# Kernel optimization log

Measured on AMD Instinct MI355X. Metric: run time of the kernel, lower is better.

## Reference

```python
import jax, jax.numpy as jnp
import numpy as np

EPS = 1e-08

def setup_inputs() -> dict:
    key = jax.random.key(0)
    ks = jax.random.split(key, 5)
    B, T, D, L = 8, 4096, 1024, 24
    data = jax.random.normal(ks[0], (B, T, D), dtype=jnp.float32)
    W_enc = jax.random.normal(ks[1], (L, D), dtype=jnp.float32) * (1.0 / np.sqrt(D))
    b_enc = jax.random.normal(ks[2], (L,), dtype=jnp.float32) * 0.01
    W_dec = jax.random.normal(ks[3], (D, L), dtype=jnp.float32) * (1.0 / np.sqrt(L))
    b_dec = jax.random.normal(ks[4], (D,), dtype=jnp.float32) * 0.01
    ecs = jnp.array([0.1], dtype=jnp.float32)  # error_correction_strength
    ep = jnp.array([1.0], dtype=jnp.float32)   # energy_preservation
    return {"data": data, "W_enc": W_enc, "b_enc": b_enc,
            "W_dec": W_dec, "b_dec": b_dec,
            "error_correction_strength": ecs, "energy_preservation": ep}

def _l2(x):
    return jnp.linalg.norm(x, axis=-1, keepdims=True)

def reference(data, W_enc, b_enc, W_dec, b_dec, error_correction_strength, energy_preservation):
    ecs = error_correction_strength[0]
    ep = energy_preservation[0]
    # --- encode_to_lattice ---
    in_e = _l2(data)                                   # [B,T,1]
    proj = jnp.einsum('btd,ld->btl', data, W_enc) + b_enc
    lattice_points = jnp.round(proj / ecs) * ecs       # quantize to lattice grid
    out_e = _l2(lattice_points)
    lattice = lattice_points * (in_e / (out_e + EPS)) * ep
    # --- decode_from_lattice ---
    in_e2 = _l2(lattice)
    corrected = jnp.where(jnp.abs(lattice) > ecs, lattice, 0.0)
    res = jnp.einsum('btl,dl->btd', corrected, W_dec) + b_dec
    out_e2 = _l2(res)
    return res * (in_e2 / (out_e2 + EPS)) * ep
```

## Files before the change

kernel.cpp:

```cpp
#include <hip/hip_runtime.h>
#include <math.h>

#define EPS 1e-8f

__global__ void prep_all(const float* __restrict__ W_enc,
                         const float* __restrict__ Wd, const float* __restrict__ bd,
                         float* __restrict__ wt, float* __restrict__ G,
                         float* __restrict__ h, float* __restrict__ bb) {
    int b = blockIdx.x;
    int lane = threadIdx.x;
    if (b < 384) {
        int i = b * 64 + lane;
        int k = i / 24, l = i - k * 24;
        wt[i] = W_enc[l * 1024 + k];
        return;
    }
    b -= 384;
    float s = 0.f;
    if (b < 576) {
        int l = b / 24, m = b - (b / 24) * 24;
        for (int d = lane; d < 1024; d += 64) s = fmaf(Wd[d * 24 + l], Wd[d * 24 + m], s);
    } else if (b < 600) {
        int l = b - 576;
        for (int d = lane; d < 1024; d += 64) s = fmaf(Wd[d * 24 + l], bd[d], s);
    } else {
        for (int d = lane; d < 1024; d += 64) s = fmaf(bd[d], bd[d], s);
    }
    for (int off = 32; off; off >>= 1) s += __shfl_down(s, off);
    if (lane == 0) {
        if (b < 576) G[b] = s;
        else if (b < 600) h[b - 576] = s;
        else *bb = s;
    }
}


constexpr int LD_TILE = 33;
constexpr int TILE_F  = 64 * LD_TILE;
constexpr int SMEM_F  = 4 * TILE_F;

__global__ __launch_bounds__(256, 4)
void leech_main(const float* __restrict__ data,
                const float* __restrict__ b_enc,
                const float* __restrict__ Wd,
                const float* __restrict__ b_dec,
                const float* __restrict__ ecs_p,
                const float* __restrict__ ep_p,
                const float* __restrict__ wt,
                const float* __restrict__ G,
                const float* __restrict__ h,
                const float* __restrict__ bbp,
                float* __restrict__ out)
{
    __shared__ float smem[SMEM_F];
    const int tid = threadIdx.x;
    const int w = tid >> 6;
    const int r = tid & 63;
    const int rowbase = blockIdx.x * 64;

    float* tile = smem + w * TILE_F;

    const int lrow = r >> 3;
    const int lk   = (r & 7) * 4;

    float proj[24];
#pragma unroll
    for (int l = 0; l < 24; ++l) proj[l] = 0.f;
    float ssq = 0.f;

    const int kw = __builtin_amdgcn_readfirstlane((tid >> 6) * 256);

    float4 buf[8];
#pragma unroll
    for (int it = 0; it < 8; ++it)
        buf[it] = *reinterpret_cast<const float4*>(
            data + (size_t)(rowbase + it * 8 + lrow) * 1024 + kw + lk);

    for (int sc = 0; sc < 8; ++sc) {
#pragma unroll
        for (int it = 0; it < 8; ++it) {
            float* t = tile + (it * 8 + lrow) * LD_TILE + lk;
            t[0] = buf[it].x; t[1] = buf[it].y; t[2] = buf[it].z; t[3] = buf[it].w;
        }
        if (sc < 7) {
            const int k0n = kw + (sc + 1) * 32;
#pragma unroll
            for (int it = 0; it < 8; ++it)
                buf[it] = *reinterpret_cast<const float4*>(
                    data + (size_t)(rowbase + it * 8 + lrow) * 1024 + k0n + lk);
        }
        const float* xrow = tile + r * LD_TILE;
        const int kofs = __builtin_amdgcn_readfirstlane(kw + sc * 32);
#pragma unroll 8
        for (int kk = 0; kk < 32; ++kk) {
            const float x = xrow[kk];
            ssq = fmaf(x, x, ssq);
            const float* wp = wt + (size_t)(kofs + kk) * 24;
#pragma unroll
            for (int l = 0; l < 24; ++l)
                proj[l] = fmaf(wp[l], x, proj[l]);
        }
    }

#pragma unroll
    for (int l = 0; l < 24; ++l)
        smem[w * TILE_F + l * 64 + r] = proj[l];
    smem[w * TILE_F + 24 * 64 + r] = ssq;
    __syncthreads();

    float p[24];
#pragma unroll
    for (int l = 0; l < 24; ++l)
        p[l] = (smem[0 * TILE_F + l * 64 + r] + smem[1 * TILE_F + l * 64 + r]) +
               (smem[2 * TILE_F + l * 64 + r] + smem[3 * TILE_F + l * 64 + r]);
    const float ss = (smem[0 * TILE_F + 24 * 64 + r] + smem[1 * TILE_F + 24 * 64 + r]) +
                     (smem[2 * TILE_F + 24 * 64 + r] + smem[3 * TILE_F + 24 * 64 + r]);
    __syncthreads();

    const float ecs = ecs_p[0];
    const float ep  = ep_p[0];
    const float in_e = sqrtf(ss);

    float lp[24]; float oe = 0.f;
#pragma unroll
    for (int l = 0; l < 24; ++l) {
        const float pp = p[l] + b_enc[l];
        const float q = rintf(pp / ecs) * ecs;
        lp[l] = q;
        oe = fmaf(q, q, oe);
    }
    const float s1 = in_e / (sqrtf(oe) + EPS) * ep;

    float c[24]; float ie = 0.f;
#pragma unroll
    for (int l = 0; l < 24; ++l) {
        const float lat = lp[l] * s1;
        ie = fmaf(lat, lat, ie);
        c[l] = (fabsf(lat) > ecs) ? lat : 0.f;
    }
    const float in_e2 = sqrtf(ie);

    float qacc = bbp[0];
#pragma unroll
    for (int l = 0; l < 24; ++l) {
        float s = 2.f * h[l];
#pragma unroll
        for (int m = 0; m < 24; ++m)
            s = fmaf(G[l * 24 + m], c[m], s);
        qacc = fmaf(s, c[l], qacc);
    }
    const float out_e2 = sqrtf(fmaxf(qacc, 0.f));
    const float s2 = in_e2 / (out_e2 + EPS) * ep;

    for (int sc = 0; sc < 8; ++sc) {
        const int d0 = __builtin_amdgcn_readfirstlane(kw + sc * 32);
        float* trow = tile + r * LD_TILE;
#pragma unroll 4
        for (int dd = 0; dd < 32; ++dd) {
            const int d = d0 + dd;
            const float* wr = Wd + d * 24;
            float acc = b_dec[d];
#pragma unroll
            for (int l = 0; l < 24; ++l)
                acc = fmaf(wr[l], c[l], acc);
            trow[dd] = acc * s2;
        }
#pragma unroll
        for (int it = 0; it < 8; ++it) {
            const float* t = tile + (it * 8 + lrow) * LD_TILE + lk;
            float4 v; v.x = t[0]; v.y = t[1]; v.z = t[2]; v.w = t[3];
            *reinterpret_cast<float4*>(
                out + (size_t)(rowbase + it * 8 + lrow) * 1024 + d0 + lk) = v;
        }
    }
}


extern "C" void kernel_launch(void* const* d_in, const int* in_sizes, int n_in,
                              void* d_out, int out_size, void* d_ws, size_t ws_size,
                              hipStream_t stream) {
    const float* data  = (const float*)d_in[0];
    const float* W_enc = (const float*)d_in[1];
    const float* b_enc = (const float*)d_in[2];
    const float* W_dec = (const float*)d_in[3];
    const float* b_dec = (const float*)d_in[4];
    const float* ecs   = (const float*)d_in[5];
    const float* ep    = (const float*)d_in[6];
    float* out = (float*)d_out;

    float* ws = (float*)d_ws;
    float* wt = ws;
    float* G  = ws + 24576;
    float* h  = ws + 25152;
    float* bb = ws + 25176;

    const int rows = in_sizes[0] / 1024;

    hipLaunchKernelGGL(prep_all, dim3(985), dim3(64), 0, stream,
                       W_enc, W_dec, b_dec, wt, G, h, bb);
    hipLaunchKernelGGL(leech_main, dim3(rows / 64), dim3(256), 0, stream,
                       data, b_enc, W_dec, b_dec, ecs, ep, wt, G, h, bb, out);
}
```

Baseline: 324.4 us.

## Split rows across eight waves, XOR-swizzle LDS tiles, use nontemporal output stores

Each 64-row block now uses 8 waves of 512 threads, with each wave covering 128 columns instead of 256. This halves the per-wave serial K loop and the decode loop, at the cost of a bigger cross-wave reduction. The padded LDS tile (stride 33) becomes an unpadded stride-32 tile with an XOR swizzle to avoid bank conflicts while keeping the footprint small. Output stores become nontemporal to avoid polluting the cache with streamed results. Launch bounds of 512x4 may raise register pressure given the 24-element accumulators.

```diff
diff --git a/kernel.cpp b/kernel.cpp
--- a/kernel.cpp
+++ b/kernel.cpp
@@ -2,6 +2,8 @@
 #include <math.h>
 
 #define EPS 1e-8f
+
+typedef float vfloat4 __attribute__((ext_vector_type(4)));
 
 __global__ void prep_all(const float* __restrict__ W_enc,
                          const float* __restrict__ Wd, const float* __restrict__ bd,
@@ -35,11 +37,12 @@
 }
 
 
-constexpr int LD_TILE = 33;
+constexpr int LD_TILE = 32;
 constexpr int TILE_F  = 64 * LD_TILE;
-constexpr int SMEM_F  = 4 * TILE_F;
-
-__global__ __launch_bounds__(256, 4)
+constexpr int NW      = 8;
+constexpr int SMEM_F  = NW * TILE_F;
+
+__global__ __launch_bounds__(512, 4)
 void leech_main(const float* __restrict__ data,
                 const float* __restrict__ b_enc,
                 const float* __restrict__ Wd,
@@ -68,7 +71,7 @@
     for (int l = 0; l < 24; ++l) proj[l] = 0.f;
     float ssq = 0.f;
 
-    const int kw = __builtin_amdgcn_readfirstlane((tid >> 6) * 256);
+    const int kw = __builtin_amdgcn_readfirstlane((tid >> 6) * 128);
 
     float4 buf[8];
 #pragma unroll
@@ -76,13 +79,18 @@
         buf[it] = *reinterpret_cast<const float4*>(
             data + (size_t)(rowbase + it * 8 + lrow) * 1024 + kw + lk);
 
-    for (int sc = 0; sc < 8; ++sc) {
+    for (int sc = 0; sc < 4; ++sc) {
 #pragma unroll
         for (int it = 0; it < 8; ++it) {
-            float* t = tile + (it * 8 + lrow) * LD_TILE + lk;
-            t[0] = buf[it].x; t[1] = buf[it].y; t[2] = buf[it].z; t[3] = buf[it].w;
-        }
-        if (sc < 7) {
+            const int row = it * 8 + lrow;
+            const int rb = row & 31;
+            float* t = tile + row * LD_TILE;
+            t[(lk + 0) ^ rb] = buf[it].x;
+            t[(lk + 1) ^ rb] = buf[it].y;
+            t[(lk + 2) ^ rb] = buf[it].z;
+            t[(lk + 3) ^ rb] = buf[it].w;
+        }
+        if (sc < 3) {
             const int k0n = kw + (sc + 1) * 32;
 #pragma unroll
             for (int it = 0; it < 8; ++it)
@@ -90,10 +98,11 @@
                     data + (size_t)(rowbase + it * 8 + lrow) * 1024 + k0n + lk);
         }
         const float* xrow = tile + r * LD_TILE;
+        const int rb = r & 31;
         const int kofs = __builtin_amdgcn_readfirstlane(kw + sc * 32);
 #pragma unroll 8
         for (int kk = 0; kk < 32; ++kk) {
-            const float x = xrow[kk];
+            const float x = xrow[kk ^ rb];
             ssq = fmaf(x, x, ssq);
             const float* wp = wt + (size_t)(kofs + kk) * 24;
 #pragma unroll
@@ -110,11 +119,21 @@
 
     float p[24];
 #pragma unroll
-    for (int l = 0; l < 24; ++l)
-        p[l] = (smem[0 * TILE_F + l * 64 + r] + smem[1 * TILE_F + l * 64 + r]) +
-               (smem[2 * TILE_F + l * 64 + r] + smem[3 * TILE_F + l * 64 + r]);
-    const float ss = (smem[0 * TILE_F + 24 * 64 + r] + smem[1 * TILE_F + 24 * 64 + r]) +
-                     (smem[2 * TILE_F + 24 * 64 + r] + smem[3 * TILE_F + 24 * 64 + r]);
+    for (int l = 0; l < 24; ++l) {
+        float s0 = smem[0 * TILE_F + l * 64 + r] + smem[1 * TILE_F + l * 64 + r];
+        float s1 = smem[2 * TILE_F + l * 64 + r] + smem[3 * TILE_F + l * 64 + r];
+        float s2 = smem[4 * TILE_F + l * 64 + r] + smem[5 * TILE_F + l * 64 + r];
+        float s3 = smem[6 * TILE_F + l * 64 + r] + smem[7 * TILE_F + l * 64 + r];
+        p[l] = (s0 + s1) + (s2 + s3);
+    }
+    float ss;
+    {
+        float s0 = smem[0 * TILE_F + 24 * 64 + r] + smem[1 * TILE_F + 24 * 64 + r];
+        float s1 = smem[2 * TILE_F + 24 * 64 + r] + smem[3 * TILE_F + 24 * 64 + r];
+        float s2 = smem[4 * TILE_F + 24 * 64 + r] + smem[5 * TILE_F + 24 * 64 + r];
+        float s3 = smem[6 * TILE_F + 24 * 64 + r] + smem[7 * TILE_F + 24 * 64 + r];
+        ss = (s0 + s1) + (s2 + s3);
+    }
     __syncthreads();
 
     const float ecs = ecs_p[0];
@@ -152,9 +171,10 @@
     const float out_e2 = sqrtf(fmaxf(qacc, 0.f));
     const float s2 = in_e2 / (out_e2 + EPS) * ep;
 
-    for (int sc = 0; sc < 8; ++sc) {
+    for (int sc = 0; sc < 4; ++sc) {
         const int d0 = __builtin_amdgcn_readfirstlane(kw + sc * 32);
         float* trow = tile + r * LD_TILE;
+        const int rb = r & 31;
 #pragma unroll 4
         for (int dd = 0; dd < 32; ++dd) {
             const int d = d0 + dd;
@@ -163,14 +183,20 @@
 #pragma unroll
             for (int l = 0; l < 24; ++l)
                 acc = fmaf(wr[l], c[l], acc);
-            trow[dd] = acc * s2;
+            trow[dd ^ rb] = acc * s2;
         }
 #pragma unroll
         for (int it = 0; it < 8; ++it) {
-            const float* t = tile + (it * 8 + lrow) * LD_TILE + lk;
-            float4 v; v.x = t[0]; v.y = t[1]; v.z = t[2]; v.w = t[3];
-            *reinterpret_cast<float4*>(
-                out + (size_t)(rowbase + it * 8 + lrow) * 1024 + d0 + lk) = v;
+            const int row = it * 8 + lrow;
+            const int rb2 = row & 31;
+            const float* t = tile + row * LD_TILE;
+            vfloat4 v;
+            v.x = t[(lk + 0) ^ rb2];
+            v.y = t[(lk + 1) ^ rb2];
+            v.z = t[(lk + 2) ^ rb2];
+            v.w = t[(lk + 3) ^ rb2];
+            __builtin_nontemporal_store(v, reinterpret_cast<vfloat4*>(
+                out + (size_t)(rowbase + row) * 1024 + d0 + lk));
         }
     }
 }
@@ -198,6 +224,6 @@
 
     hipLaunchKernelGGL(prep_all, dim3(985), dim3(64), 0, stream,
                        W_enc, W_dec, b_dec, wt, G, h, bb);
-    hipLaunchKernelGGL(leech_main, dim3(rows / 64), dim3(256), 0, stream,
+    hipLaunchKernelGGL(leech_main, dim3(rows / 64), dim3(512), 0, stream,
                        data, b_enc, W_dec, b_dec, ecs, ep, wt, G, h, bb, out);
 }
```

Result: faster. 312.4 us (-3.7%).
